# Optimization experiments

Measured on AMD Instinct MI355X. Metric: run time of the kernel, lower is better.

Reference implementation:

```python
import jax, jax.numpy as jnp
import numpy as np

N = 100000   # nodes
E = 1600000  # edges (avg degree 16)
D = 64       # in_dim
H = 64       # hidden_dim
NEG_SLOPE = 0.2


def setup_inputs() -> dict:
    key = jax.random.key(0)
    ks = jax.random.split(key, 10)
    s = 0.1  # param init scale
    return {
        "x": jax.random.normal(ks[0], (N, D), jnp.float32),
        "edge_index": jax.random.randint(ks[1], (2, E), 0, N, dtype=jnp.int64),
        "h": jax.random.normal(ks[2], (1, N, H), jnp.float32),
        "c": jax.random.normal(ks[3], (1, N, H), jnp.float32),
        "W_gat": jax.random.normal(ks[4], (D, H), jnp.float32) * s,
        "att_src": jax.random.normal(ks[5], (H,), jnp.float32) * s,
        "att_dst": jax.random.normal(ks[6], (H,), jnp.float32) * s,
        "bias_gat": jax.random.normal(ks[7], (H,), jnp.float32) * s,
        "W_ih": jax.random.normal(ks[8], (4 * H, H), jnp.float32) * s,
        "W_hh": jax.random.normal(ks[9], (4 * H, H), jnp.float32) * s,
    }


def reference(x, edge_index, h, c, W_gat, att_src, att_dst, bias_gat, W_ih, W_hh):
    src, dst = edge_index[0], edge_index[1]  # message j -> i

    # ---- Breadth: GATConv (heads=1) + tanh ----
    xs = x @ W_gat                             # [N, H] projected features
    a_src = xs @ att_src                       # [N]
    a_dst = xs @ att_dst                       # [N]
    e = jax.nn.leaky_relu(a_src[src] + a_dst[dst], NEG_SLOPE)  # [E]
    # scatter-softmax over incoming edges of each destination node
    m = jax.lax.stop_gradient(jax.ops.segment_max(e, dst, num_segments=N))
    p = jnp.exp(e - m[dst])
    z = jax.ops.segment_sum(p, dst, num_segments=N)
    alpha = p / (z[dst] + 1e-16)               # [E]
    agg = jax.ops.segment_sum(xs[src] * alpha[:, None], dst, num_segments=N)
    xb = jnp.tanh(agg + bias_gat)              # [N, H]

    # ---- Depth: single-step bias-free LSTM ----
    h0, c0 = h[0], c[0]                        # [N, H]
    gates = xb @ W_ih.T + h0 @ W_hh.T          # [N, 4H]
    i, f, g, o = jnp.split(gates, 4, axis=-1)  # torch gate order i,f,g,o
    c1 = jax.nn.sigmoid(f) * c0 + jax.nn.sigmoid(i) * jnp.tanh(g)
    h1 = jax.nn.sigmoid(o) * jnp.tanh(c1)
    return h1, h1[None], c1[None]
```

## Files before the change

### kernel.cpp

```cpp
#include <hip/hip_runtime.h>
#include <cmath>

#define NN 100000
#define EE 1600000
#define NB 1563
#define CAP 1344
#define EPB 25

using bf16x8 = __attribute__((ext_vector_type(8))) __bf16;
using f32x4  = __attribute__((ext_vector_type(4))) float;

__device__ __forceinline__ unsigned short f2bf(float f) {
  __bf16 b = (__bf16)f;
  return __builtin_bit_cast(unsigned short, b);
}
__device__ __forceinline__ float bflo(unsigned int u) {
  return __uint_as_float(u << 16);
}
__device__ __forceinline__ float bfhi(unsigned int u) {
  return __uint_as_float(u & 0xffff0000u);
}
__device__ __forceinline__ float sigmoidf_(float v) {
  return 1.0f / (1.0f + __expf(-v));
}
__device__ __forceinline__ float tanhfast(float v) {
  return 1.0f - 2.0f / (1.0f + __expf(2.0f * v));
}
__device__ __forceinline__ bf16x8 cvt8(float4 a, float4 b) {
  bf16x8 r;
  r[0]=(__bf16)a.x; r[1]=(__bf16)a.y; r[2]=(__bf16)a.z; r[3]=(__bf16)a.w;
  r[4]=(__bf16)b.x; r[5]=(__bf16)b.y; r[6]=(__bf16)b.z; r[7]=(__bf16)b.w;
  return r;
}

__global__ __launch_bounds__(128) void k_prep(
    const float* __restrict__ Wih, const float* __restrict__ Whh,
    const float* __restrict__ Wg,
    unsigned short* __restrict__ wperm, unsigned short* __restrict__ wgp)
{
  if (blockIdx.x < 256) {
    const int p = blockIdx.x, k = threadIdx.x;
    const int g = p & 3;
    const int h = (p >> 4) + ((p >> 2) & 3) * 16;
    const int row = g*64 + h;
    const float v = (k < 64) ? Wih[row*64 + k] : Whh[row*64 + (k - 64)];
    wperm[p*128 + k] = f2bf(v);
  } else {
    for (int idx = threadIdx.x; idx < 4096; idx += 128) {
      const int lane = idx >> 6, r = idx & 63;
      const int nt = r >> 4, kf = (r >> 3) & 1, j = r & 7;
      const int m = lane & 15, quad = lane >> 4;
      wgp[idx] = f2bf(Wg[(kf*32 + quad*8 + j)*64 + nt*16 + m]);
    }
  }
}

__global__ __launch_bounds__(256) void k_binproj(
    const int* __restrict__ ei, int* __restrict__ bcursor,
    unsigned int* __restrict__ binned,
    const float* __restrict__ x, const unsigned short* __restrict__ wgp,
    const float* __restrict__ att_s, const float* __restrict__ att_d,
    unsigned short* __restrict__ xs16, float* __restrict__ a_src,
    float* __restrict__ a_dst)
{
  if (blockIdx.x < 256) {
    __shared__ int cnt[NB];
    __shared__ int gbase[NB];
    const int tid = threadIdx.x;
    const size_t base = (size_t)blockIdx.x * 256 * EPB;

    for (int b = tid; b < NB; b += 256) cnt[b] = 0;
    __syncthreads();

    unsigned int pay[EPB];
    int bidx[EPB], pos[EPB];
    #pragma unroll
    for (int j = 0; j < EPB; ++j) {
      const size_t e = base + (size_t)j*256 + tid;
      if (e < EE) {
        const int s = ei[e];
        const int d = ei[EE + e];
        bidx[j] = d >> 6;
        pay[j] = (unsigned)s | ((unsigned)(d & 63) << 17);
        pos[j] = atomicAdd(&cnt[bidx[j]], 1);
      } else {
        bidx[j] = -1;
      }
    }
    __syncthreads();

    for (int b = tid; b < NB; b += 256) {
      const int c = cnt[b];
      gbase[b] = c ? atomicAdd(&bcursor[b*16], c) : 0;
    }
    __syncthreads();

    #pragma unroll
    for (int j = 0; j < EPB; ++j) {
      if (bidx[j] >= 0) {
        const int g = gbase[bidx[j]] + pos[j];
        if (g < CAP) binned[(size_t)bidx[j]*CAP + g] = pay[j];
      }
    }
  } else {
    const int lane = threadIdx.x & 63;
    const int wave = threadIdx.x >> 6;
    const int tile = (blockIdx.x - 256) * 4 + wave;
    if (tile >= NN / 16) return;
    const int m = lane & 15, quad = lane >> 4;

    bf16x8 bfrag[4][2];
    {
      const unsigned short* wp = wgp + lane*64;
      #pragma unroll
      for (int nt = 0; nt < 4; ++nt)
        #pragma unroll
        for (int kf = 0; kf < 2; ++kf)
          bfrag[nt][kf] = *(const bf16x8*)(wp + nt*16 + kf*8);
    }

    const int row = tile*16 + m;
    bf16x8 afrag[2];
    #pragma unroll
    for (int kf = 0; kf < 2; ++kf) {
      const float4* p = (const float4*)(x + (size_t)row*64 + kf*32 + quad*8);
      afrag[kf] = cvt8(p[0], p[1]);
    }

    f32x4 acc[4];
    #pragma unroll
    for (int nt = 0; nt < 4; ++nt) acc[nt] = f32x4{0.f, 0.f, 0.f, 0.f};
    #pragma unroll
    for (int nt = 0; nt < 4; ++nt)
      #pragma unroll
      for (int kf = 0; kf < 2; ++kf)
        acc[nt] = __builtin_amdgcn_mfma_f32_16x16x32_bf16(
            afrag[kf], bfrag[nt][kf], acc[nt], 0, 0, 0);

    float ss[4] = {0.f,0.f,0.f,0.f}, sd[4] = {0.f,0.f,0.f,0.f};
    #pragma unroll
    for (int nt = 0; nt < 4; ++nt) {
      const float av = att_s[nt*16 + m], dv = att_d[nt*16 + m];
      #pragma unroll
      for (int r = 0; r < 4; ++r) {
        const float v = acc[nt][r];
        xs16[(size_t)(tile*16 + quad*4 + r)*64 + nt*16 + m] = f2bf(v);
        ss[r] += v * av;
        sd[r] += v * dv;
      }
    }
    #pragma unroll
    for (int off = 1; off < 16; off <<= 1) {
      #pragma unroll
      for (int r = 0; r < 4; ++r) {
        ss[r] += __shfl_xor(ss[r], off);
        sd[r] += __shfl_xor(sd[r], off);
      }
    }
    if (m == 0) {
      #pragma unroll
      for (int r = 0; r < 4; ++r) {
        a_src[tile*16 + quad*4 + r] = ss[r];
        a_dst[tile*16 + quad*4 + r] = sd[r];
      }
    }
  }
}

__global__ __launch_bounds__(256) void k_agg(
    const int* __restrict__ bcursor, const unsigned int* __restrict__ binned,
    const float* __restrict__ a_src, const float* __restrict__ a_dst,
    const unsigned short* __restrict__ xs16, const float* __restrict__ bias,
    const unsigned short* __restrict__ wperm, const float* __restrict__ h0,
    const float* __restrict__ c0, float* __restrict__ out)
{
  __shared__ unsigned int raw[CAP];
  __shared__ unsigned int csr[CAP];
  __shared__ int cnt[64], offs[64], cursor[64];
  __shared__ unsigned short xb_lds[64*64];
  const int b = blockIdx.x;
  const int tid = threadIdx.x;
  const int ne = min(bcursor[b*16], CAP);

  if (tid < 64) cnt[tid] = 0;
  __syncthreads();
  for (int i = tid; i < ne; i += 256) {
    const unsigned int w = binned[(size_t)b*CAP + i];
    raw[i] = w;
    atomicAdd(&cnt[(w >> 17) & 63], 1);
  }
  __syncthreads();
  if (tid < 64) {
    const int v = cnt[tid];
    int inc = v;
    #pragma unroll
    for (int dd = 1; dd < 64; dd <<= 1) {
      const int o = __shfl_up(inc, dd, 64);
      if (tid >= dd) inc += o;
    }
    offs[tid] = inc - v;
    cursor[tid] = inc - v;
  }
  __syncthreads();
  for (int i = tid; i < ne; i += 256) {
    const unsigned int w = raw[i];
    const int pos = atomicAdd(&cursor[(w >> 17) & 63], 1);
    csr[pos] = w;
  }
  __syncthreads();

  const int lane = tid & 63;
  const int wv = tid >> 6;
  const int grp = lane >> 4, l16 = lane & 15;
  const float4 b4 = *(const float4*)(bias + l16*4);
  for (int t = 0; t < 16; ++t) {
    const int nl = wv*16 + t;
    const int node = b*64 + nl;
    if (node >= NN) break;
    const int bse = offs[nl];
    const int dg = cnt[nl];
    const float ad = a_dst[node];
    float acc0=0.f, acc1=0.f, acc2=0.f, acc3=0.f, psum=0.f;
    for (int e = grp; e < dg; e += 4) {
      const int s = (int)(csr[bse + e] & 0x1FFFFu);
      float ev = a_src[s] + ad;
      ev = (ev >= 0.f) ? ev : 0.2f*ev;
      const float pv = __expf(ev);
      const uint2 rw = *(const uint2*)(xs16 + (size_t)s*64 + l16*4);
      psum += pv;
      acc0 += pv*bflo(rw.x); acc1 += pv*bfhi(rw.x);
      acc2 += pv*bflo(rw.y); acc3 += pv*bfhi(rw.y);
    }
    #pragma unroll
    for (int off = 16; off < 64; off <<= 1) {
      acc0 += __shfl_xor(acc0, off);
      acc1 += __shfl_xor(acc1, off);
      acc2 += __shfl_xor(acc2, off);
      acc3 += __shfl_xor(acc3, off);
      psum += __shfl_xor(psum, off);
    }
    if (lane < 16) {
      const float invz = 1.f/(psum + 1e-16f);
      ushort4 o;
      o.x = f2bf(tanhfast(acc0*invz + b4.x));
      o.y = f2bf(tanhfast(acc1*invz + b4.y));
      o.z = f2bf(tanhfast(acc2*invz + b4.z));
      o.w = f2bf(tanhfast(acc3*invz + b4.w));
      *(ushort4*)(xb_lds + nl*64 + (((l16*4)) ^ ((nl & 7) << 3))) = o;
    }
  }
  __syncthreads();

  const int m = l16;
  const int quad = grp;
  bf16x8 wfr[4][4];
  #pragma unroll
  for (int u = 0; u < 4; ++u) {
    const unsigned short* wr = wperm + (size_t)((wv*4 + u)*16 + m)*128;
    #pragma unroll
    for (int kf = 0; kf < 4; ++kf)
      wfr[u][kf] = *(const bf16x8*)(wr + kf*32 + quad*8);
  }

  #pragma unroll
  for (int nt = 0; nt < 4; ++nt) {
    if (b*64 + nt*16 >= NN) break;
    const int row = nt*16 + m;
    const int node = b*64 + row;
    const int sw = (row & 7) << 3;
    bf16x8 bfr[4];
    bfr[0] = *(const bf16x8*)(xb_lds + row*64 + ((      quad*8) ^ sw));
    bfr[1] = *(const bf16x8*)(xb_lds + row*64 + ((32 + quad*8) ^ sw));
    {
      const float* p0 = h0 + (size_t)node*64 + quad*8;
      bfr[2] = cvt8(*(const float4*)p0, *(const float4*)(p0 + 4));
      const float* p1 = h0 + (size_t)node*64 + 32 + quad*8;
      bfr[3] = cvt8(*(const float4*)p1, *(const float4*)(p1 + 4));
    }

    f32x4 acc[4];
    #pragma unroll
    for (int u = 0; u < 4; ++u) acc[u] = f32x4{0.f, 0.f, 0.f, 0.f};
    #pragma unroll
    for (int u = 0; u < 4; ++u)
      #pragma unroll
      for (int kf = 0; kf < 4; ++kf)
        acc[u] = __builtin_amdgcn_mfma_f32_16x16x32_bf16(
            wfr[u][kf], bfr[kf], acc[u], 0, 0, 0);

    const size_t obase = (size_t)node*64 + quad*16 + wv*4;
    const float4 cv = *(const float4*)(c0 + obase);
    const float cvv[4] = {cv.x, cv.y, cv.z, cv.w};
    float h1a[4], c1a[4];
    #pragma unroll
    for (int u = 0; u < 4; ++u) {
      const float gi = acc[u][0], gf = acc[u][1];
      const float gg = acc[u][2], go = acc[u][3];
      const float c1 = sigmoidf_(gf)*cvv[u] + sigmoidf_(gi)*tanhfast(gg);
      h1a[u] = sigmoidf_(go)*tanhfast(c1);
      c1a[u] = c1;
    }
    const float4 hv  = make_float4(h1a[0], h1a[1], h1a[2], h1a[3]);
    const float4 c1v = make_float4(c1a[0], c1a[1], c1a[2], c1a[3]);
    *(float4*)(out + obase) = hv;
    *(float4*)(out + (size_t)NN*64 + obase) = hv;
    *(float4*)(out + (size_t)2*NN*64 + obase) = c1v;
  }
}

extern "C" void kernel_launch(void* const* d_in, const int* in_sizes, int n_in,
                              void* d_out, int out_size, void* d_ws, size_t ws_size,
                              hipStream_t stream) {
  const float* x    = (const float*)d_in[0];
  const int*   ei   = (const int*)d_in[1];
  const float* h    = (const float*)d_in[2];
  const float* c    = (const float*)d_in[3];
  const float* Wg   = (const float*)d_in[4];
  const float* atts = (const float*)d_in[5];
  const float* attd = (const float*)d_in[6];
  const float* bg   = (const float*)d_in[7];
  const float* Wih  = (const float*)d_in[8];
  const float* Whh  = (const float*)d_in[9];
  float* out = (float*)d_out;

  char* w = (char*)d_ws;
  unsigned short* xs16  = (unsigned short*)w; w += (size_t)NN*64*2;
  unsigned short* wperm = (unsigned short*)w; w += (size_t)256*128*2;
  unsigned short* wgp   = (unsigned short*)w; w += (size_t)4096*2;
  unsigned int*   binned= (unsigned int*)w;  w += (size_t)NB*CAP*4;
  float* a_src = (float*)w; w += (size_t)NN*4;
  float* a_dst = (float*)w; w += (size_t)NN*4;
  int* bcursor = (int*)w;   w += (size_t)NB*16*4;

  hipMemsetAsync(bcursor, 0, (size_t)NB*16*4, stream);

  k_prep    <<<257, 128, 0, stream>>>(Wih, Whh, Wg, wperm, wgp);
  k_binproj <<<256 + (NN/16 + 3)/4, 256, 0, stream>>>(
      ei, bcursor, binned, x, wgp, atts, attd, xs16, a_src, a_dst);
  k_agg     <<<NB, 256, 0, stream>>>(
      bcursor, binned, a_src, a_dst, xs16, bg, wperm, h, c, out);
}
```

Baseline: 320.0 us.

## Split fused aggregation+LSTM kernel into separate agg and LSTM kernels

Measured after the change: 305.6 us. 4.5% less time.

```diff
diff --git a/kernel.cpp b/kernel.cpp
--- a/kernel.cpp
+++ b/kernel.cpp
@@ -171,13 +171,11 @@
     const int* __restrict__ bcursor, const unsigned int* __restrict__ binned,
     const float* __restrict__ a_src, const float* __restrict__ a_dst,
     const unsigned short* __restrict__ xs16, const float* __restrict__ bias,
-    const unsigned short* __restrict__ wperm, const float* __restrict__ h0,
-    const float* __restrict__ c0, float* __restrict__ out)
+    unsigned short* __restrict__ xb16)
 {
   __shared__ unsigned int raw[CAP];
   __shared__ unsigned int csr[CAP];
   __shared__ int cnt[64], offs[64], cursor[64];
-  __shared__ unsigned short xb_lds[64*64];
   const int b = blockIdx.x;
   const int tid = threadIdx.x;
   const int ne = min(bcursor[b*16], CAP);
@@ -246,13 +244,20 @@
       o.y = f2bf(tanhfast(acc1*invz + b4.y));
       o.z = f2bf(tanhfast(acc2*invz + b4.z));
       o.w = f2bf(tanhfast(acc3*invz + b4.w));
-      *(ushort4*)(xb_lds + nl*64 + (((l16*4)) ^ ((nl & 7) << 3))) = o;
-    }
-  }
-  __syncthreads();
-
-  const int m = l16;
-  const int quad = grp;
+      *(ushort4*)(xb16 + (size_t)node*64 + l16*4) = o;
+    }
+  }
+}
+
+__global__ __launch_bounds__(256) void k_lstm(
+    const unsigned short* __restrict__ xb16, const float* __restrict__ h0,
+    const float* __restrict__ c0, const unsigned short* __restrict__ wperm,
+    float* __restrict__ out)
+{
+  const int lane = threadIdx.x & 63;
+  const int wv = threadIdx.x >> 6;
+  const int m = lane & 15, quad = lane >> 4;
+
   bf16x8 wfr[4][4];
   #pragma unroll
   for (int u = 0; u < 4; ++u) {
@@ -262,15 +267,14 @@
       wfr[u][kf] = *(const bf16x8*)(wr + kf*32 + quad*8);
   }
 
-  #pragma unroll
-  for (int nt = 0; nt < 4; ++nt) {
-    if (b*64 + nt*16 >= NN) break;
-    const int row = nt*16 + m;
-    const int node = b*64 + row;
-    const int sw = (row & 7) << 3;
+  for (int tile = blockIdx.x; tile < NN/16; tile += gridDim.x) {
+    const int node = tile*16 + m;
+    const size_t obase = (size_t)node*64 + quad*16 + wv*4;
+    const float4 cv = *(const float4*)(c0 + obase);
+
     bf16x8 bfr[4];
-    bfr[0] = *(const bf16x8*)(xb_lds + row*64 + ((      quad*8) ^ sw));
-    bfr[1] = *(const bf16x8*)(xb_lds + row*64 + ((32 + quad*8) ^ sw));
+    bfr[0] = *(const bf16x8*)(xb16 + (size_t)node*64 + quad*8);
+    bfr[1] = *(const bf16x8*)(xb16 + (size_t)node*64 + 32 + quad*8);
     {
       const float* p0 = h0 + (size_t)node*64 + quad*8;
       bfr[2] = cvt8(*(const float4*)p0, *(const float4*)(p0 + 4));
@@ -288,8 +292,6 @@
         acc[u] = __builtin_amdgcn_mfma_f32_16x16x32_bf16(
             wfr[u][kf], bfr[kf], acc[u], 0, 0, 0);
 
-    const size_t obase = (size_t)node*64 + quad*16 + wv*4;
-    const float4 cv = *(const float4*)(c0 + obase);
     const float cvv[4] = {cv.x, cv.y, cv.z, cv.w};
     float h1a[4], c1a[4];
     #pragma unroll
@@ -325,6 +327,7 @@
 
   char* w = (char*)d_ws;
   unsigned short* xs16  = (unsigned short*)w; w += (size_t)NN*64*2;
+  unsigned short* xb16  = (unsigned short*)w; w += (size_t)NN*64*2;
   unsigned short* wperm = (unsigned short*)w; w += (size_t)256*128*2;
   unsigned short* wgp   = (unsigned short*)w; w += (size_t)4096*2;
   unsigned int*   binned= (unsigned int*)w;  w += (size_t)NB*CAP*4;
@@ -337,6 +340,6 @@
   k_prep    <<<257, 128, 0, stream>>>(Wih, Whh, Wg, wperm, wgp);
   k_binproj <<<256 + (NN/16 + 3)/4, 256, 0, stream>>>(
       ei, bcursor, binned, x, wgp, atts, attd, xs16, a_src, a_dst);
-  k_agg     <<<NB, 256, 0, stream>>>(
-      bcursor, binned, a_src, a_dst, xs16, bg, wperm, h, c, out);
-}
+  k_agg     <<<NB, 256, 0, stream>>>(bcursor, binned, a_src, a_dst, xs16, bg, xb16);
+  k_lstm    <<<2084, 256, 0, stream>>>(xb16, h, c, wperm, out);
+}
```
